# Performance work log

Hardware: AMD Instinct MI355X
Metric: run time of the kernel (lower is better)

The kernel has to match this reference:

```python
import jax, jax.numpy as jnp
import numpy as np

DIM = 384
HEADS = 12
WIN = (2, 7, 7)
MLP_RATIO = 4.0
EPS = 1e-5


def _rel_index(Wt, Wh, Ww):
    t, h, w = np.meshgrid(np.arange(Wt), np.arange(Wh), np.arange(Ww), indexing='ij')
    coords = np.stack([t, h, w]).reshape(3, -1).T  # (N,3)
    rel = coords[:, None] - coords[None]  # (N,N,3)
    rel[..., 0] += Wt - 1
    rel[..., 1] += Wh - 1
    rel[..., 2] += Ww - 1
    rel[..., 0] *= (2 * Wh - 1) * (2 * Ww - 1)
    rel[..., 1] *= (2 * Ww - 1)
    return rel.sum(-1)  # (N,N) int


def setup_inputs() -> dict:
    key = jax.random.key(0)
    ks = jax.random.split(key, 16)
    d = DIM
    hdim = int(d * MLP_RATIO)
    Wt, Wh, Ww = WIN
    table_size = (2 * Wt - 1) * (2 * Wh - 1) * (2 * Ww - 1)
    s = lambda fan: 1.0 / np.sqrt(fan)
    return {
        'x': jax.random.normal(ks[0], (2, 8, 56, 56, d), jnp.float32),
        'norm1_g': jnp.ones((d,), jnp.float32),
        'norm1_b': jnp.zeros((d,), jnp.float32),
        'qkv_w': jax.random.normal(ks[1], (d, 3 * d), jnp.float32) * s(d),
        'qkv_b': jnp.zeros((3 * d,), jnp.float32),
        'proj_w': jax.random.normal(ks[2], (d, d), jnp.float32) * s(d),
        'proj_b': jnp.zeros((d,), jnp.float32),
        'bias_table': jax.random.normal(ks[3], (table_size, HEADS), jnp.float32) * 0.02,
        'norm2_g': jnp.ones((d,), jnp.float32),
        'norm2_b': jnp.zeros((d,), jnp.float32),
        'fc1_w': jax.random.normal(ks[4], (d, hdim), jnp.float32) * s(d),
        'fc1_b': jnp.zeros((hdim,), jnp.float32),
        'fc2_w': jax.random.normal(ks[5], (hdim, d), jnp.float32) * s(hdim),
        'fc2_b': jnp.zeros((d,), jnp.float32),
        'rel_index': jnp.asarray(_rel_index(*WIN), jnp.int32),
    }


def _ln(x, g, b):
    mu = x.mean(-1, keepdims=True)
    var = ((x - mu) ** 2).mean(-1, keepdims=True)
    return (x - mu) * jax.lax.rsqrt(var + EPS) * g + b


def _window_partition(x, win):
    B, T, H, W, C = x.shape
    Wt, Wh, Ww = win
    x = x.reshape(B, T // Wt, Wt, H // Wh, Wh, W // Ww, Ww, C)
    x = x.transpose(0, 1, 3, 5, 2, 4, 6, 7)
    return x.reshape(-1, Wt * Wh * Ww, C)


def _window_reverse(win_x, win, B, T, H, W):
    Wt, Wh, Ww = win
    C = win_x.shape[-1]
    x = win_x.reshape(B, T // Wt, H // Wh, W // Ww, Wt, Wh, Ww, C)
    x = x.transpose(0, 1, 4, 2, 5, 3, 6, 7)
    return x.reshape(B, T, H, W, C)


def reference(x, norm1_g, norm1_b, qkv_w, qkv_b, proj_w, proj_b, bias_table,
              norm2_g, norm2_b, fc1_w, fc1_b, fc2_w, fc2_b, rel_index):
    B, T, H, W, C = x.shape
    Wt, Wh, Ww = WIN
    N = Wt * Wh * Ww
    shift = (Wt // 2, Wh // 2, Ww // 2)
    head_dim = C // HEADS
    scale = head_dim ** -0.5

    shortcut = x
    h = _ln(x, norm1_g, norm1_b)
    h = jnp.roll(h, shift=(-shift[0], -shift[1], -shift[2]), axis=(1, 2, 3))
    # dims chosen divisible by window -> no padding branch
    wins = _window_partition(h, WIN)  # (BnW, N, C)
    BnW = wins.shape[0]

    qkv = wins @ qkv_w + qkv_b  # (BnW, N, 3C)
    qkv = qkv.reshape(BnW, N, 3, HEADS, head_dim).transpose(2, 0, 3, 1, 4)
    q, k, v = qkv[0] * scale, qkv[1], qkv[2]  # (BnW, H, N, d)

    bias = bias_table[rel_index.reshape(-1)].reshape(N, N, HEADS).transpose(2, 0, 1)
    attn = jnp.einsum('bhnd,bhmd->bhnm', q, k) + bias[None]
    attn = jax.nn.softmax(attn, axis=-1)
    out = jnp.einsum('bhnm,bhmd->bhnd', attn, v)
    out = out.transpose(0, 2, 1, 3).reshape(BnW, N, C)
    out = out @ proj_w + proj_b

    h = _window_reverse(out.reshape(-1, Wt, Wh, Ww, C), WIN, B, T, H, W)
    h = jnp.roll(h, shift=shift, axis=(1, 2, 3))
    x = shortcut + h

    h2 = _ln(x, norm2_g, norm2_b)
    h2 = jax.nn.gelu(h2 @ fc1_w + fc1_b, approximate=False) @ fc2_w + fc2_b
    return x + h2
```

## Files before the change

### kernel.cpp

```cpp
#include <hip/hip_runtime.h>
#include <cstdint>
#include <cstddef>


typedef __bf16 bf16x8 __attribute__((ext_vector_type(8)));
typedef __bf16 bf16x4 __attribute__((ext_vector_type(4)));
typedef float f32x4 __attribute__((ext_vector_type(4)));

#define DIM 384
#define QKV_DIM 1152
#define HID 1536
#define NHEADS 12
#define NTOK 50176
#define NWIN 512

__device__ __forceinline__ void gload16(const void* g, void* s) {
  __builtin_amdgcn_global_load_lds(
      (const __attribute__((address_space(1))) void*)g,
      (__attribute__((address_space(3))) void*)s, 16, 0, 0);
}

__global__ __launch_bounds__(256) void build_tokmap_k(int* __restrict__ map) {
  int t = blockIdx.x * 256 + threadIdx.x;
  if (t >= NTOK) return;
  int win = t / 98, n = t - win * 98;
  int b = win >> 8, tw = (win >> 6) & 3, hw = (win >> 3) & 7, ww = win & 7;
  int dt = n / 49; int rem = n - dt * 49; int dh = rem / 7, dw = rem - dh * 7;
  int t0 = (tw * 2 + dt + 1) & 7;
  int h0 = hw * 7 + dh + 3; if (h0 >= 56) h0 -= 56;
  int w0 = ww * 7 + dw + 3; if (w0 >= 56) w0 -= 56;
  map[t] = ((b * 8 + t0) * 56 + h0) * 56 + w0;
}

__global__ __launch_bounds__(256) void expand_biasp_k(const float* __restrict__ table,
                                                      const int* __restrict__ rel,
                                                      float* __restrict__ out) {
  int e = blockIdx.x * 256 + threadIdx.x;
  if (e >= NHEADS * 49 * 256) return;
  int r = e & 3, l = (e >> 2) & 63;
  int rest = e >> 8;
  int ni = rest % 7, mi = (rest / 7) % 7, h = rest / 49;
  int i = mi * 16 + (l >> 4) * 4 + r;
  int j = ni * 16 + (l & 15);
  float v;
  if (j >= 98) v = -1e30f;
  else if (i >= 98) v = 0.f;
  else v = table[rel[i * 98 + j] * NHEADS + h];
  out[e] = v;
}

__global__ __launch_bounds__(256) void pack_w64_k(const float* __restrict__ W,
                                                  __bf16* __restrict__ WP,
                                                  int K, int N, int nk,
                                                  int scaleCols, float scale) {
  int idx = blockIdx.x * 256 + threadIdx.x;
  if (idx >= (K * N) >> 3) return;
  int l = idx & 63, f = (idx >> 6) & 7;
  int rest = idx >> 9, kt = rest % nk, cn = rest / nk;
  int n = f >> 1, kk = f & 1;
  int col = cn * 64 + n * 16 + (l & 15);
  int k0 = kt * 64 + (kk * 4 + (l >> 4)) * 8;
  float sc = (col < scaleCols) ? scale : 1.0f;
  bf16x8 v;
  #pragma unroll
  for (int j = 0; j < 8; ++j)
    v[j] = (__bf16)(W[(size_t)(k0 + j) * N + col] * sc);
  *(bf16x8*)(WP + (size_t)idx * 8) = v;
}

__global__ __launch_bounds__(256) void pack_w96_k(const float* __restrict__ W,
                                                  __bf16* __restrict__ WP) {
  int idx = blockIdx.x * 256 + threadIdx.x;
  if (idx >= (HID * DIM) >> 3) return;
  int l = idx & 63, n = (idx >> 6) % 6;
  int j8 = (idx / 384) % 48, w = idx / 18432;
  int col = w * 96 + n * 16 + (l & 15);
  int k0 = j8 * 32 + (l >> 4) * 8;
  bf16x8 v;
  #pragma unroll
  for (int j = 0; j < 8; ++j)
    v[j] = (__bf16)W[(size_t)(k0 + j) * DIM + col];
  *(bf16x8*)(WP + (size_t)idx * 8) = v;
}

__global__ __launch_bounds__(256) void scale_bias_k(const float* __restrict__ b,
                                                    float* __restrict__ out,
                                                    int n, int scaleCols, float scale) {
  int e = blockIdx.x * 256 + threadIdx.x;
  if (e >= n) return;
  out[e] = b[e] * (e < scaleCols ? scale : 1.0f);
}

__global__ __launch_bounds__(384) void vtrans_k(const __bf16* __restrict__ qkv,
                                                __bf16* __restrict__ vt) {
  __shared__ __align__(1024) char T[98304];
  int win = blockIdx.x, t = threadIdx.x;
  const __bf16* base = qkv + (size_t)win * 98 * QKV_DIM + 768 + t;
  #pragma unroll
  for (int c = 0; c < 16; ++c) {
    bf16x8 pk;
    #pragma unroll
    for (int e2 = 0; e2 < 8; ++e2) {
      int tok = c * 8 + e2;
      pk[e2] = (tok < 98) ? base[(size_t)tok * QKV_DIM] : (__bf16)0.f;
    }
    *(bf16x8*)(T + t * 256 + ((c ^ (t & 15)) << 4)) = pk;
  }
  __syncthreads();
  char* wb = (char*)(vt + (size_t)win * 49152);
  #pragma unroll
  for (int i = 0; i < 16; ++i) {
    int g = i * 6144 + t * 16;
    int row = g >> 8, p = (g >> 4) & 15;
    bf16x8 v = *(const bf16x8*)(T + row * 256 + (p << 4));
    int lc = p ^ (row & 15);
    *(bf16x8*)(wb + row * 256 + (lc << 4)) = v;
  }
}

template <typename T, bool MAP>
__global__ __launch_bounds__(256) void ln_pack_k(const T* __restrict__ x,
                                                 const float* __restrict__ g,
                                                 const float* __restrict__ bta,
                                                 __bf16* __restrict__ outp,
                                                 const int* __restrict__ map) {
  const int w = threadIdx.x >> 6, l = threadIdx.x & 63;
  const int tok = blockIdx.x * 32 + w * 8 + (l >> 3);
  const int src = MAP ? map[tok] : tok;
  const T* row = x + (size_t)src * DIM;
  const int o0 = l & 7;
  float v[6][8];
  float s = 0.f;
  #pragma unroll
  for (int j = 0; j < 6; ++j) {
    const int c = (o0 + 8 * j) * 8;
    if constexpr (sizeof(T) == 4) {
      f32x4 p0 = *(const f32x4*)(row + c);
      f32x4 p1 = *(const f32x4*)(row + c + 4);
      #pragma unroll
      for (int e = 0; e < 4; ++e) { v[j][e] = p0[e]; v[j][e + 4] = p1[e]; }
    } else {
      bf16x8 p = *(const bf16x8*)(row + c);
      #pragma unroll
      for (int e = 0; e < 8; ++e) v[j][e] = (float)p[e];
    }
    #pragma unroll
    for (int e = 0; e < 8; ++e) s += v[j][e];
  }
  s += __shfl_xor(s, 1, 64); s += __shfl_xor(s, 2, 64); s += __shfl_xor(s, 4, 64);
  const float mu = s * (1.f / DIM);
  float var = 0.f;
  #pragma unroll
  for (int j = 0; j < 6; ++j)
    #pragma unroll
    for (int e = 0; e < 8; ++e) { float d = v[j][e] - mu; var += d * d; }
  var += __shfl_xor(var, 1, 64); var += __shfl_xor(var, 2, 64); var += __shfl_xor(var, 4, 64);
  const float rs = rsqrtf(var * (1.f / DIM) + 1e-5f);
  const int mg = tok >> 6, m = (tok >> 4) & 3, lr = tok & 15;
  const int kk = o0 >> 2, lg = o0 & 3;
  __bf16* dst = outp + (size_t)mg * 24576 + (m * 2 + kk) * 512 + (lg * 16 + lr) * 8;
  #pragma unroll
  for (int j = 0; j < 6; ++j) {
    const int c = (o0 + 8 * j) * 8;
    f32x4 g0 = *(const f32x4*)(g + c), g1 = *(const f32x4*)(g + c + 4);
    f32x4 b0 = *(const f32x4*)(bta + c), b1 = *(const f32x4*)(bta + c + 4);
    bf16x8 ov;
    #pragma unroll
    for (int e = 0; e < 4; ++e) {
      ov[e] = (__bf16)((v[j][e] - mu) * rs * g0[e] + b0[e]);
      ov[e + 4] = (__bf16)((v[j][e + 4] - mu) * rs * g1[e] + b1[e]);
    }
    *(bf16x8*)(dst + (size_t)j * 4096) = ov;
  }
}

template <int EPI, int NK>
__global__ __launch_bounds__(256) void gemm_stream_k(const __bf16* __restrict__ AP,
                                                     const __bf16* __restrict__ WP,
                                                     const float* __restrict__ bias,
                                                     int N,
                                                     __bf16* __restrict__ outb) {
  __shared__ __align__(1024) char lds[32768];
  const int tid = threadIdx.x;
  const int l = tid & 63, w = tid >> 6;
  const int lr = l & 15, lg = l >> 4;
  const int ntile = N >> 6;
  const int nwg = gridDim.x, qd = nwg >> 3, rm = nwg & 7;
  const int xcd = blockIdx.x & 7;
  const int wgid = (xcd < rm ? xcd * (qd + 1) : rm * (qd + 1) + (xcd - rm) * qd)
                   + (blockIdx.x >> 3);
  const int bm = wgid / ntile, bn = wgid - bm * ntile;
  const int mg = bm * 4 + w;
  const int m0 = mg << 6, n0 = bn << 6;
  const __bf16* pA = AP + (size_t)mg * (NK * 4096) + l * 8;
  const __bf16* pB = WP + (size_t)bn * (NK * 4096) + l * 8;

  bf16x8 a[2][8], b[2][8];
  f32x4 acc[4][4] = {};
  #pragma unroll
  for (int f = 0; f < 8; ++f) {
    a[0][f] = *(const bf16x8*)(pA + f * 512);
    b[0][f] = *(const bf16x8*)(pB + f * 512);
  }
  #pragma unroll
  for (int kt = 0; kt < NK; ++kt) {
    const int cur = kt & 1, nxt = cur ^ 1;
    if (kt < NK - 1) {
      const size_t ko = (size_t)(kt + 1) * 4096;
      #pragma unroll
      for (int f = 0; f < 8; ++f) {
        a[nxt][f] = *(const bf16x8*)(pA + ko + f * 512);
        b[nxt][f] = *(const bf16x8*)(pB + ko + f * 512);
      }
      asm volatile("s_waitcnt vmcnt(16)" ::: "memory");
    } else {
      asm volatile("s_waitcnt vmcnt(0)" ::: "memory");
    }
    __builtin_amdgcn_sched_barrier(0);
    __builtin_amdgcn_s_setprio(1);
    #pragma unroll
    for (int kk = 0; kk < 2; ++kk)
      #pragma unroll
      for (int m = 0; m < 4; ++m)
        #pragma unroll
        for (int n = 0; n < 4; ++n)
          acc[m][n] = __builtin_amdgcn_mfma_f32_16x16x32_bf16(
              b[cur][n * 2 + kk], a[cur][m * 2 + kk], acc[m][n], 0, 0, 0);
    __builtin_amdgcn_s_setprio(0);
  }

  char* abuf = lds + (w << 13);
  #pragma unroll
  for (int m = 0; m < 4; ++m) {
    const int row = (m << 4) + lr;
    #pragma unroll
    for (int n = 0; n < 4; ++n) {
      const int gcol = n0 + (n << 4) + (lg << 2);
      f32x4 a4 = acc[m][n] + *(const f32x4*)(bias + gcol);
      bf16x4 c;
      #pragma unroll
      for (int r = 0; r < 4; ++r) c[r] = (__bf16)a4[r];
      const int ch = (n << 1) + (lg >> 1);
      *(bf16x4*)(abuf + (row << 7) + ((ch ^ (row & 7)) << 4) + ((lg & 1) << 3)) = c;
    }
  }
  asm volatile("s_waitcnt lgkmcnt(0)" ::: "memory");
  __builtin_amdgcn_sched_barrier(0);
  #pragma unroll
  for (int i = 0; i < 8; ++i) {
    const int row = (i << 3) + (l >> 3);
    const int p = (l & 7) ^ (row & 7);
    bf16x8 v = *(const bf16x8*)(abuf + (row << 7) + (p << 4));
    *(bf16x8*)(outb + (size_t)(m0 + row) * N + n0 + ((l & 7) << 3)) = v;
  }
}

__global__ __launch_bounds__(256, 2) void mlp_fused_k(const __bf16* __restrict__ AP,
                                                      const __bf16* __restrict__ W1P,
                                                      const float* __restrict__ b1,
                                                      const __bf16* __restrict__ W2P,
                                                      const float* __restrict__ b2,
                                                      const __bf16* __restrict__ s1,
                                                      float* __restrict__ outp) {
  __shared__ __align__(1024) char lds[81920];
  const int tid = threadIdx.x, l = tid & 63, w = tid >> 6;
  const int lr = l & 15, lg = l >> 4;
  const int bid = (blockIdx.x & 7) * (gridDim.x >> 3) + (blockIdx.x >> 3);
  const int tok0 = bid << 6;

  const __bf16* APg = AP + (size_t)bid * 24576;
  #pragma unroll
  for (int i = 0; i < 12; ++i) {
    const int c = w * 12 + i;
    gload16(APg + c * 512 + l * 8, lds + c * 1024);
  }
  asm volatile("s_waitcnt vmcnt(0)" ::: "memory");
  asm volatile("s_barrier" ::: "memory");

  char* hbase = lds + 49152;
  char* hb = hbase + (w << 13);
  const __bf16* W2w = W2P + (size_t)w * 147456 + l * 8;
  f32x4 acc2[4][6] = {};

#define LOADW2(dst, j, t)                                                      \
  { _Pragma("unroll")                                                          \
    for (int q_ = 0; q_ < 2; ++q_)                                             \
      _Pragma("unroll")                                                        \
      for (int n_ = 0; n_ < 6; ++n_)                                           \
        dst[q_ * 6 + n_] = *(const bf16x8*)(                                   \
            W2w + (size_t)(((j) * 8 + 2 * (t) + q_) * 6 + n_) * 512); }
#define FC2_STEP(T, BCUR, BNXT)                                                \
  {                                                                            \
    if ((T) < 3) LOADW2(BNXT, j, (T) + 1)                                      \
    bf16x8 ah[4][2];                                                           \
    const char* ht = hbase + ((T) << 13);                                      \
    _Pragma("unroll")                                                          \
    for (int m_ = 0; m_ < 4; ++m_)                                             \
      _Pragma("unroll")                                                        \
      for (int q_ = 0; q_ < 2; ++q_) {                                         \
        const int r_ = (m_ << 4) + lr, ck_ = (q_ << 2) + lg;                   \
        ah[m_][q_] = *(const bf16x8*)(ht + (r_ << 7) + ((ck_ ^ (r_ & 7)) << 4)); \
      }                                                                        \
    __builtin_amdgcn_s_setprio(1);                                             \
    _Pragma("unroll")                                                          \
    for (int q_ = 0; q_ < 2; ++q_)                                             \
      _Pragma("unroll")                                                        \
      for (int m_ = 0; m_ < 4; ++m_)                                           \
        _Pragma("unroll")                                                      \
        for (int n_ = 0; n_ < 6; ++n_)                                         \
          acc2[m_][n_] = __builtin_amdgcn_mfma_f32_16x16x32_bf16(              \
              BCUR[q_ * 6 + n_], ah[m_][q_], acc2[m_][n_], 0, 0, 0);           \
    __builtin_amdgcn_s_setprio(0);                                             \
  }

  for (int j = 0; j < 6; ++j) {
    const int g = j * 4 + w;
    const __bf16* W1g = W1P + (size_t)g * 24576 + l * 8;
    f32x4 acc1[4][4] = {};
    #pragma unroll
    for (int kt = 0; kt < 6; ++kt) {
      bf16x8 a[4][2], b[8];
      #pragma unroll
      for (int f = 0; f < 8; ++f)
        b[f] = *(const bf16x8*)(W1g + kt * 4096 + f * 512);
      #pragma unroll
      for (int m = 0; m < 4; ++m)
        #pragma unroll
        for (int kk = 0; kk < 2; ++kk)
          a[m][kk] = *(const bf16x8*)(lds + (kt * 8 + m * 2 + kk) * 1024 + l * 16);
      __builtin_amdgcn_s_setprio(1);
      #pragma unroll
      for (int kk = 0; kk < 2; ++kk)
        #pragma unroll
        for (int m = 0; m < 4; ++m)
          #pragma unroll
          for (int n = 0; n < 4; ++n)
            acc1[m][n] = __builtin_amdgcn_mfma_f32_16x16x32_bf16(
                b[n * 2 + kk], a[m][kk], acc1[m][n], 0, 0, 0);
      __builtin_amdgcn_s_setprio(0);
    }
    asm volatile("s_barrier" ::: "memory");
    #pragma unroll
    for (int m = 0; m < 4; ++m) {
      const int row = (m << 4) + lr;
      #pragma unroll
      for (int n = 0; n < 4; ++n) {
        f32x4 a4 = acc1[m][n] + *(const f32x4*)(b1 + g * 64 + (n << 4) + (lg << 2));
        bf16x4 c;
        #pragma unroll
        for (int r = 0; r < 4; ++r) {
          float vv = a4[r];
          float y = vv * (1.0f + 0.044715f * vv * vv);
          c[r] = (__bf16)(vv / (1.0f + __expf(-1.5957691216057308f * y)));
        }
        const int ch = (n << 1) + (lg >> 1);
        *(bf16x4*)(hb + (row << 7) + ((ch ^ (row & 7)) << 4) + ((lg & 1) << 3)) = c;
      }
    }
    asm volatile("s_waitcnt lgkmcnt(0)" ::: "memory");
    __builtin_amdgcn_sched_barrier(0);
    asm volatile("s_barrier" ::: "memory");
    {
      bf16x8 bhA[12], bhB[12];
      LOADW2(bhA, j, 0)
      FC2_STEP(0, bhA, bhB)
      FC2_STEP(1, bhB, bhA)
      FC2_STEP(2, bhA, bhB)
      FC2_STEP(3, bhB, bhA)
    }
  }
#undef FC2_STEP
#undef LOADW2

  const int col0 = w * 96;
  #pragma unroll
  for (int m = 0; m < 4; ++m) {
    const int grow = tok0 + (m << 4) + lr;
    #pragma unroll
    for (int n = 0; n < 6; ++n) {
      const int gcol = col0 + (n << 4) + (lg << 2);
      f32x4 a4 = acc2[m][n] + *(const f32x4*)(b2 + gcol);
      bf16x4 sv = *(const bf16x4*)(s1 + (size_t)grow * DIM + gcol);
      f32x4 o;
      #pragma unroll
      for (int r = 0; r < 4; ++r) o[r] = a4[r] + (float)sv[r];
      *(f32x4*)(outp + (size_t)grow * DIM + gcol) = o;
    }
  }
}

__global__ __launch_bounds__(256) void gemm_proj_k(const __bf16* __restrict__ A,
                                                   const __bf16* __restrict__ WP,
                                                   const float* __restrict__ bias,
                                                   int M, int N, int K,
                                                   __bf16* __restrict__ outb,
                                                   const float* __restrict__ residf,
                                                   const int* __restrict__ tokmap) {
  __shared__ __align__(1024) char lds[32768];
  const int tid = threadIdx.x;
  const int l = tid & 63, w = tid >> 6;
  const int lr = l & 15, lg = l >> 4;
  const int ntile = N >> 6;
  const int nwg = gridDim.x, qd = nwg >> 3, rm = nwg & 7;
  const int xcd = blockIdx.x & 7;
  const int wgid = (xcd < rm ? xcd * (qd + 1) : rm * (qd + 1) + (xcd - rm) * qd)
                   + (blockIdx.x >> 3);
  const int bm = wgid / ntile, bn = wgid - bm * ntile;
  const int m0 = (bm << 8) + (w << 6);
  const int n0 = bn << 6;
  const int nk = K >> 6;
  const int sch = (l & 7) ^ ((l >> 3) & 7);
  const __bf16* pa = A + (size_t)(m0 + (l >> 3)) * K + sch * 8;
  char* abuf = lds + (w << 13);
  const __bf16* pB = WP + (size_t)bn * nk * 4096 + l * 8;

#define STAGEA(kt)                                                   \
  { const size_t ko_ = (size_t)(kt) << 6;                            \
    _Pragma("unroll")                                                \
    for (int s_ = 0; s_ < 8; ++s_)                                   \
      gload16(pa + (size_t)(s_ * 8) * K + ko_, abuf + s_ * 1024); }
#define LOADB(kt)                                                    \
  { const __bf16* p_ = pB + (size_t)(kt) * 4096;                     \
    _Pragma("unroll")                                                \
    for (int f_ = 0; f_ < 8; ++f_)                                   \
      b[f_] = *(const bf16x8*)(p_ + f_ * 512); }
#define LDA()                                                        \
  { _Pragma("unroll")                                                \
    for (int kk_ = 0; kk_ < 2; ++kk_) {                              \
      const int ck_ = (kk_ << 2) + lg;                               \
      _Pragma("unroll")                                              \
      for (int m_ = 0; m_ < 4; ++m_) {                               \
        int r_ = (m_ << 4) + lr;                                     \
        a[m_][kk_] = *(const bf16x8*)(abuf + (r_ << 7) +             \
                                      ((ck_ ^ (r_ & 7)) << 4));      \
      } }                                                            \
    asm volatile("s_waitcnt lgkmcnt(0)" ::: "memory");               \
    __builtin_amdgcn_sched_barrier(0); }

  bf16x8 a[4][2], b[8];
  f32x4 acc[4][4] = {};
  STAGEA(0)
  asm volatile("s_waitcnt vmcnt(0)" ::: "memory");
  LDA()
  for (int kt = 0; kt < nk; ++kt) {
    LOADB(kt)
    const bool pf = (kt + 1 < nk);
    if (pf) STAGEA(kt + 1)
    __builtin_amdgcn_s_setprio(1);
    #pragma unroll
    for (int kk = 0; kk < 2; ++kk)
      #pragma unroll
      for (int m = 0; m < 4; ++m)
        #pragma unroll
        for (int n = 0; n < 4; ++n)
          acc[m][n] = __builtin_amdgcn_mfma_f32_16x16x32_bf16(b[n * 2 + kk], a[m][kk],
                                                              acc[m][n], 0, 0, 0);
    __builtin_amdgcn_s_setprio(0);
    if (pf) {
      asm volatile("s_waitcnt vmcnt(0)" ::: "memory");
      LDA()
    }
  }
#undef STAGEA
#undef LOADB
#undef LDA

  #pragma unroll
  for (int m = 0; m < 4; ++m) {
    const int row = (m << 4) + lr;
    #pragma unroll
    for (int n = 0; n < 4; ++n) {
      const int gcol = n0 + (n << 4) + (lg << 2);
      f32x4 a4 = acc[m][n] + *(const f32x4*)(bias + gcol);
      bf16x4 c;
      #pragma unroll
      for (int r = 0; r < 4; ++r) c[r] = (__bf16)a4[r];
      const int ch = (n << 1) + (lg >> 1);
      *(bf16x4*)(abuf + (row << 7) + ((ch ^ (row & 7)) << 4) + ((lg & 1) << 3)) = c;
    }
  }
  asm volatile("s_waitcnt lgkmcnt(0)" ::: "memory");
  __builtin_amdgcn_sched_barrier(0);
  #pragma unroll
  for (int i = 0; i < 8; ++i) {
    const int row = (i << 3) + (l >> 3);
    const int p = (l & 7) ^ (row & 7);
    bf16x8 v = *(const bf16x8*)(abuf + (row << 7) + (p << 4));
    const int gcol = n0 + ((l & 7) << 3);
    const int dst = tokmap[m0 + row];
    const float* rp = residf + (size_t)dst * N + gcol;
    f32x4 r0 = *(const f32x4*)rp, r1 = *(const f32x4*)(rp + 4);
    bf16x8 c2;
    #pragma unroll
    for (int j = 0; j < 4; ++j) {
      c2[j] = (__bf16)(r0[j] + (float)v[j]);
      c2[j + 4] = (__bf16)(r1[j] + (float)v[j + 4]);
    }
    *(bf16x8*)(outb + (size_t)dst * N + gcol) = c2;
  }
}

__global__ __launch_bounds__(64) void attn_k(const __bf16* __restrict__ qkv,
                                             const __bf16* __restrict__ vt,
                                             const float* __restrict__ pb,
                                             __bf16* __restrict__ out) {
  __shared__ __align__(1024) char P[4096];
  const int l = threadIdx.x, lr = l & 15, lg = l >> 4;
  const int bid = blockIdx.x;
  const int xc = bid & 7, kk = bid >> 3;
  const int wh = (kk / 7) * 8 + xc, mi = kk % 7;
  const int win = wh / NHEADS, h = wh - win * NHEADS;
  const size_t wbase = (size_t)win * 98 * QKV_DIM;
  const __bf16* qb = qkv + wbase + h * 32;
  const __bf16* kb = qb + 384;
  const bf16x8 z8 = {};
  const f32x4 fz = {};

  bf16x8 kf[7];
  #pragma unroll
  for (int ni = 0; ni < 7; ++ni) {
    int tok = ni * 16 + lr;
    kf[ni] = (tok < 98) ? *(const bf16x8*)(kb + (size_t)tok * QKV_DIM + lg * 8) : z8;
  }
  int qt = mi * 16 + lr;
  bf16x8 qf = (qt < 98) ? *(const bf16x8*)(qb + (size_t)qt * QKV_DIM + lg * 8) : z8;
  const f32x4* pbp = (const f32x4*)pb + (size_t)((h * 7 + mi) * 7) * 64 + l;
  f32x4 bv[7];
  #pragma unroll
  for (int ni = 0; ni < 7; ++ni) bv[ni] = pbp[ni * 64];

  f32x4 s[7];
  #pragma unroll
  for (int ni = 0; ni < 7; ++ni)
    s[ni] = __builtin_amdgcn_mfma_f32_16x16x32_bf16(qf, kf[ni], fz, 0, 0, 0);

  if (l < 32) {
    int row = l >> 1, c = 14 + (l & 1);
    *(f32x4*)(P + row * 256 + ((c ^ (row & 7)) << 4)) = fz;
  }

  #pragma unroll
  for (int r = 0; r < 4; ++r) {
    float mx = -1e30f;
    #pragma unroll
    for (int ni = 0; ni < 7; ++ni) {
      float vv = s[ni][r] + bv[ni][r];
      s[ni][r] = vv;
      mx = fmaxf(mx, vv);
    }
    #pragma unroll
    for (int m2 = 1; m2 < 16; m2 <<= 1) mx = fmaxf(mx, __shfl_xor(mx, m2, 64));
    float sum = 0.f;
    #pragma unroll
    for (int ni = 0; ni < 7; ++ni) { float p = __expf(s[ni][r] - mx); s[ni][r] = p; sum += p; }
    #pragma unroll
    for (int m2 = 1; m2 < 16; m2 <<= 1) sum += __shfl_xor(sum, m2, 64);
    float inv = 1.0f / sum;
    int il = lg * 4 + r;
    #pragma unroll
    for (int ni = 0; ni < 7; ++ni) {
      int j = ni * 16 + lr;
      *(__bf16*)(P + il * 256 + (((j >> 3) ^ (il & 7)) << 4) + ((j & 7) << 1)) =
          (__bf16)(s[ni][r] * inv);
    }
  }
  __syncthreads();

  bf16x8 pa[4];
  #pragma unroll
  for (int ks = 0; ks < 4; ++ks) {
    int ck = ks * 4 + lg;
    pa[ks] = *(const bf16x8*)(P + lr * 256 + ((ck ^ (lr & 7)) << 4));
  }
  const __bf16* vrow = vt + ((size_t)wh * 32) * 128;
  f32x4 oo[2];
  #pragma unroll
  for (int nf = 0; nf < 2; ++nf) {
    int d = nf * 16 + lr;
    f32x4 o = fz;
    #pragma unroll
    for (int ks = 0; ks < 4; ++ks) {
      bf16x8 vb = *(const bf16x8*)(vrow + (size_t)d * 128 + ks * 32 + lg * 8);
      o = __builtin_amdgcn_mfma_f32_16x16x32_bf16(pa[ks], vb, o, 0, 0, 0);
    }
    oo[nf] = o;
  }
  #pragma unroll
  for (int nf = 0; nf < 2; ++nf)
    #pragma unroll
    for (int r = 0; r < 4; ++r)
      *(__bf16*)(P + (lg * 4 + r) * 64 + (((nf << 4) + lr) << 1)) = (__bf16)oo[nf][r];
  asm volatile("s_waitcnt lgkmcnt(0)" ::: "memory");
  __builtin_amdgcn_sched_barrier(0);
  {
    const int row = l >> 2;
    bf16x8 v = *(const bf16x8*)(P + row * 64 + ((l & 3) << 4));
    const int tok = mi * 16 + row;
    if (tok < 98)
      *(bf16x8*)(out + ((size_t)win * 98 + tok) * DIM + h * 32 + ((l & 3) << 3)) = v;
  }
}

extern "C" void kernel_launch(void* const* d_in, const int* in_sizes, int n_in,
                              void* d_out, int out_size, void* d_ws, size_t ws_size,
                              hipStream_t stream) {
  const float* x      = (const float*)d_in[0];
  const float* n1g    = (const float*)d_in[1];
  const float* n1b    = (const float*)d_in[2];
  const float* qkv_w  = (const float*)d_in[3];
  const float* qkv_b  = (const float*)d_in[4];
  const float* proj_w = (const float*)d_in[5];
  const float* proj_b = (const float*)d_in[6];
  const float* btab   = (const float*)d_in[7];
  const float* n2g    = (const float*)d_in[8];
  const float* n2b    = (const float*)d_in[9];
  const float* fc1_w  = (const float*)d_in[10];
  const float* fc1_b  = (const float*)d_in[11];
  const float* fc2_w  = (const float*)d_in[12];
  const float* fc2_b  = (const float*)d_in[13];
  const int*   relidx = (const int*)d_in[14];
  float* outp = (float*)d_out;
  (void)in_sizes; (void)n_in; (void)out_size; (void)ws_size;

  char* ws = (char*)d_ws;
  size_t off = 0;
  auto alloc = [&](size_t bytes) {
    char* p = ws + off;
    off = (off + bytes + 255) & ~(size_t)255;
    return p;
  };
  int*    tokmap  = (int*)alloc((size_t)NTOK * 4);
  float*  biasex  = (float*)alloc((size_t)NHEADS * 49 * 256 * 4);
  __bf16* wqkvP   = (__bf16*)alloc((size_t)QKV_DIM * DIM * 2);
  __bf16* wprojP  = (__bf16*)alloc((size_t)DIM * DIM * 2);
  __bf16* wfc1P   = (__bf16*)alloc((size_t)HID * DIM * 2);
  __bf16* wfc2P   = (__bf16*)alloc((size_t)DIM * HID * 2);
  float*  qkvbS   = (float*)alloc((size_t)QKV_DIM * 4);
  __bf16* tokens  = (__bf16*)alloc((size_t)NTOK * DIM * 2);
  __bf16* qkvbuf  = (__bf16*)alloc((size_t)NTOK * HID * 2);
  __bf16* s1      = (__bf16*)alloc((size_t)NTOK * DIM * 2);
  __bf16* tokens2 = (__bf16*)alloc((size_t)NTOK * DIM * 2);
  __bf16* attnout = tokens;
  __bf16* vt = (__bf16*)d_out;

  const float scale = 0.17677669529663687f;

  build_tokmap_k<<<NTOK / 256, 256, 0, stream>>>(tokmap);
  expand_biasp_k<<<(NHEADS * 49 * 256) / 256, 256, 0, stream>>>(btab, relidx, biasex);
  pack_w64_k<<<(DIM * QKV_DIM / 8) / 256, 256, 0, stream>>>(qkv_w, wqkvP, DIM, QKV_DIM, 6, DIM, scale);
  pack_w64_k<<<(DIM * DIM / 8) / 256, 256, 0, stream>>>(proj_w, wprojP, DIM, DIM, 6, 0, 1.0f);
  pack_w64_k<<<(DIM * HID / 8) / 256, 256, 0, stream>>>(fc1_w, wfc1P, DIM, HID, 6, 0, 1.0f);
  pack_w96_k<<<(HID * DIM / 8) / 256, 256, 0, stream>>>(fc2_w, wfc2P);
  scale_bias_k<<<(QKV_DIM + 255) / 256, 256, 0, stream>>>(qkv_b, qkvbS, QKV_DIM, DIM, scale);

  ln_pack_k<float, true><<<NTOK / 32, 256, 0, stream>>>(x, n1g, n1b, tokens, tokmap);
  gemm_stream_k<0, 6><<<(NTOK / 256) * (QKV_DIM / 64), 256, 0, stream>>>(
      tokens, wqkvP, qkvbS, QKV_DIM, qkvbuf);
  vtrans_k<<<NWIN, 384, 0, stream>>>(qkvbuf, vt);
  attn_k<<<NWIN * NHEADS * 7, 64, 0, stream>>>(qkvbuf, vt, biasex, attnout);
  gemm_proj_k<<<(NTOK / 256) * (DIM / 64), 256, 0, stream>>>(
      attnout, wprojP, proj_b, NTOK, DIM, DIM, s1, x, tokmap);
  ln_pack_k<__bf16, false><<<NTOK / 32, 256, 0, stream>>>(s1, n2g, n2b, tokens2, nullptr);
  mlp_fused_k<<<NTOK / 64, 256, 0, stream>>>(
      tokens2, wfc1P, fc1_b, wfc2P, fc2_b, s1, outp);
}
```

Baseline: 450.6 us.

## Fuse LN2 into MLP kernel and write attention output in packed GEMM layout

The attention kernel now writes its output directly in the pre-packed tile layout that the streaming GEMM consumes. This lets the projection reuse gemm_stream_k with a residual-scatter epilogue instead of the separate gemm_proj_k that staged A through LDS. The standalone second LayerNorm pack kernel is removed: mlp_fused_k reads s1 rows, computes mean and variance, and writes the normalized bf16 tile straight into LDS. This saves one kernel launch and a full-size write and read of the intermediate tensor, at the cost of extra register pressure and latency in the MLP prologue.

```diff
diff --git a/kernel.cpp b/kernel.cpp
--- a/kernel.cpp
+++ b/kernel.cpp
@@ -179,7 +179,9 @@
                                                      const __bf16* __restrict__ WP,
                                                      const float* __restrict__ bias,
                                                      int N,
-                                                     __bf16* __restrict__ outb) {
+                                                     __bf16* __restrict__ outb,
+                                                     const float* __restrict__ residf,
+                                                     const int* __restrict__ tokmap) {
   __shared__ __align__(1024) char lds[32768];
   const int tid = threadIdx.x;
   const int l = tid & 63, w = tid >> 6;
@@ -251,16 +253,31 @@
     const int row = (i << 3) + (l >> 3);
     const int p = (l & 7) ^ (row & 7);
     bf16x8 v = *(const bf16x8*)(abuf + (row << 7) + (p << 4));
-    *(bf16x8*)(outb + (size_t)(m0 + row) * N + n0 + ((l & 7) << 3)) = v;
-  }
-}
-
-__global__ __launch_bounds__(256, 2) void mlp_fused_k(const __bf16* __restrict__ AP,
+    const int gcol = n0 + ((l & 7) << 3);
+    if (EPI == 1) {
+      const int dst = tokmap[m0 + row];
+      const float* rp = residf + (size_t)dst * N + gcol;
+      f32x4 r0 = *(const f32x4*)rp, r1 = *(const f32x4*)(rp + 4);
+      bf16x8 c2;
+      #pragma unroll
+      for (int j = 0; j < 4; ++j) {
+        c2[j] = (__bf16)(r0[j] + (float)v[j]);
+        c2[j + 4] = (__bf16)(r1[j] + (float)v[j + 4]);
+      }
+      *(bf16x8*)(outb + (size_t)dst * N + gcol) = c2;
+    } else {
+      *(bf16x8*)(outb + (size_t)(m0 + row) * N + gcol) = v;
+    }
+  }
+}
+
+__global__ __launch_bounds__(256, 2) void mlp_fused_k(const __bf16* __restrict__ s1,
+                                                      const float* __restrict__ g2,
+                                                      const float* __restrict__ bt2,
                                                       const __bf16* __restrict__ W1P,
                                                       const float* __restrict__ b1,
                                                       const __bf16* __restrict__ W2P,
                                                       const float* __restrict__ b2,
-                                                      const __bf16* __restrict__ s1,
                                                       float* __restrict__ outp) {
   __shared__ __align__(1024) char lds[81920];
   const int tid = threadIdx.x, l = tid & 63, w = tid >> 6;
@@ -268,14 +285,47 @@
   const int bid = (blockIdx.x & 7) * (gridDim.x >> 3) + (blockIdx.x >> 3);
   const int tok0 = bid << 6;
 
-  const __bf16* APg = AP + (size_t)bid * 24576;
-  #pragma unroll
-  for (int i = 0; i < 12; ++i) {
-    const int c = w * 12 + i;
-    gload16(APg + c * 512 + l * 8, lds + c * 1024);
-  }
-  asm volatile("s_waitcnt vmcnt(0)" ::: "memory");
-  asm volatile("s_barrier" ::: "memory");
+  {
+    const int rloc = (w << 4) + (l >> 2);
+    const int p = l & 3;
+    const __bf16* srow = s1 + (size_t)(tok0 + rloc) * DIM;
+    float vv[12][8];
+    float s = 0.f;
+    #pragma unroll
+    for (int j = 0; j < 12; ++j) {
+      const int o = (j << 2) + p;
+      bf16x8 pk = *(const bf16x8*)(srow + (o << 3));
+      #pragma unroll
+      for (int e = 0; e < 8; ++e) { vv[j][e] = (float)pk[e]; s += vv[j][e]; }
+    }
+    s += __shfl_xor(s, 1, 64); s += __shfl_xor(s, 2, 64);
+    const float mu = s * (1.f / DIM);
+    float var = 0.f;
+    #pragma unroll
+    for (int j = 0; j < 12; ++j)
+      #pragma unroll
+      for (int e = 0; e < 8; ++e) { float d = vv[j][e] - mu; var += d * d; }
+    var += __shfl_xor(var, 1, 64); var += __shfl_xor(var, 2, 64);
+    const float rs = rsqrtf(var * (1.f / DIM) + 1e-5f);
+    const int m2 = rloc >> 4, lr2 = rloc & 15;
+    #pragma unroll
+    for (int j = 0; j < 12; ++j) {
+      const int o = (j << 2) + p;
+      const int kt = o >> 3, kk2 = (o >> 2) & 1, lg2 = o & 3;
+      f32x4 g0 = *(const f32x4*)(g2 + (o << 3));
+      f32x4 g1 = *(const f32x4*)(g2 + (o << 3) + 4);
+      f32x4 b0 = *(const f32x4*)(bt2 + (o << 3));
+      f32x4 b1 = *(const f32x4*)(bt2 + (o << 3) + 4);
+      bf16x8 ov;
+      #pragma unroll
+      for (int e = 0; e < 4; ++e) {
+        ov[e] = (__bf16)((vv[j][e] - mu) * rs * g0[e] + b0[e]);
+        ov[e + 4] = (__bf16)((vv[j][e + 4] - mu) * rs * g1[e] + b1[e]);
+      }
+      *(bf16x8*)(lds + (kt * 8 + m2 * 2 + kk2) * 1024 + ((lg2 << 4) + lr2) * 16) = ov;
+    }
+  }
+  __syncthreads();
 
   char* hbase = lds + 49152;
   char* hb = hbase + (w << 13);
@@ -349,9 +399,9 @@
         bf16x4 c;
         #pragma unroll
         for (int r = 0; r < 4; ++r) {
-          float vv = a4[r];
-          float y = vv * (1.0f + 0.044715f * vv * vv);
-          c[r] = (__bf16)(vv / (1.0f + __expf(-1.5957691216057308f * y)));
+          float vvv = a4[r];
+          float y = vvv * (1.0f + 0.044715f * vvv * vvv);
+          c[r] = (__bf16)(vvv / (1.0f + __expf(-1.5957691216057308f * y)));
         }
         const int ch = (n << 1) + (lg >> 1);
         *(bf16x4*)(hb + (row << 7) + ((ch ^ (row & 7)) << 4) + ((lg & 1) << 3)) = c;
@@ -389,121 +439,10 @@
   }
 }
 
-__global__ __launch_bounds__(256) void gemm_proj_k(const __bf16* __restrict__ A,
-                                                   const __bf16* __restrict__ WP,
-                                                   const float* __restrict__ bias,
-                                                   int M, int N, int K,
-                                                   __bf16* __restrict__ outb,
-                                                   const float* __restrict__ residf,
-                                                   const int* __restrict__ tokmap) {
-  __shared__ __align__(1024) char lds[32768];
-  const int tid = threadIdx.x;
-  const int l = tid & 63, w = tid >> 6;
-  const int lr = l & 15, lg = l >> 4;
-  const int ntile = N >> 6;
-  const int nwg = gridDim.x, qd = nwg >> 3, rm = nwg & 7;
-  const int xcd = blockIdx.x & 7;
-  const int wgid = (xcd < rm ? xcd * (qd + 1) : rm * (qd + 1) + (xcd - rm) * qd)
-                   + (blockIdx.x >> 3);
-  const int bm = wgid / ntile, bn = wgid - bm * ntile;
-  const int m0 = (bm << 8) + (w << 6);
-  const int n0 = bn << 6;
-  const int nk = K >> 6;
-  const int sch = (l & 7) ^ ((l >> 3) & 7);
-  const __bf16* pa = A + (size_t)(m0 + (l >> 3)) * K + sch * 8;
-  char* abuf = lds + (w << 13);
-  const __bf16* pB = WP + (size_t)bn * nk * 4096 + l * 8;
-
-#define STAGEA(kt)                                                   \
-  { const size_t ko_ = (size_t)(kt) << 6;                            \
-    _Pragma("unroll")                                                \
-    for (int s_ = 0; s_ < 8; ++s_)                                   \
-      gload16(pa + (size_t)(s_ * 8) * K + ko_, abuf + s_ * 1024); }
-#define LOADB(kt)                                                    \
-  { const __bf16* p_ = pB + (size_t)(kt) * 4096;                     \
-    _Pragma("unroll")                                                \
-    for (int f_ = 0; f_ < 8; ++f_)                                   \
-      b[f_] = *(const bf16x8*)(p_ + f_ * 512); }
-#define LDA()                                                        \
-  { _Pragma("unroll")                                                \
-    for (int kk_ = 0; kk_ < 2; ++kk_) {                              \
-      const int ck_ = (kk_ << 2) + lg;                               \
-      _Pragma("unroll")                                              \
-      for (int m_ = 0; m_ < 4; ++m_) {                               \
-        int r_ = (m_ << 4) + lr;                                     \
-        a[m_][kk_] = *(const bf16x8*)(abuf + (r_ << 7) +             \
-                                      ((ck_ ^ (r_ & 7)) << 4));      \
-      } }                                                            \
-    asm volatile("s_waitcnt lgkmcnt(0)" ::: "memory");               \
-    __builtin_amdgcn_sched_barrier(0); }
-
-  bf16x8 a[4][2], b[8];
-  f32x4 acc[4][4] = {};
-  STAGEA(0)
-  asm volatile("s_waitcnt vmcnt(0)" ::: "memory");
-  LDA()
-  for (int kt = 0; kt < nk; ++kt) {
-    LOADB(kt)
-    const bool pf = (kt + 1 < nk);
-    if (pf) STAGEA(kt + 1)
-    __builtin_amdgcn_s_setprio(1);
-    #pragma unroll
-    for (int kk = 0; kk < 2; ++kk)
-      #pragma unroll
-      for (int m = 0; m < 4; ++m)
-        #pragma unroll
-        for (int n = 0; n < 4; ++n)
-          acc[m][n] = __builtin_amdgcn_mfma_f32_16x16x32_bf16(b[n * 2 + kk], a[m][kk],
-                                                              acc[m][n], 0, 0, 0);
-    __builtin_amdgcn_s_setprio(0);
-    if (pf) {
-      asm volatile("s_waitcnt vmcnt(0)" ::: "memory");
-      LDA()
-    }
-  }
-#undef STAGEA
-#undef LOADB
-#undef LDA
-
-  #pragma unroll
-  for (int m = 0; m < 4; ++m) {
-    const int row = (m << 4) + lr;
-    #pragma unroll
-    for (int n = 0; n < 4; ++n) {
-      const int gcol = n0 + (n << 4) + (lg << 2);
-      f32x4 a4 = acc[m][n] + *(const f32x4*)(bias + gcol);
-      bf16x4 c;
-      #pragma unroll
-      for (int r = 0; r < 4; ++r) c[r] = (__bf16)a4[r];
-      const int ch = (n << 1) + (lg >> 1);
-      *(bf16x4*)(abuf + (row << 7) + ((ch ^ (row & 7)) << 4) + ((lg & 1) << 3)) = c;
-    }
-  }
-  asm volatile("s_waitcnt lgkmcnt(0)" ::: "memory");
-  __builtin_amdgcn_sched_barrier(0);
-  #pragma unroll
-  for (int i = 0; i < 8; ++i) {
-    const int row = (i << 3) + (l >> 3);
-    const int p = (l & 7) ^ (row & 7);
-    bf16x8 v = *(const bf16x8*)(abuf + (row << 7) + (p << 4));
-    const int gcol = n0 + ((l & 7) << 3);
-    const int dst = tokmap[m0 + row];
-    const float* rp = residf + (size_t)dst * N + gcol;
-    f32x4 r0 = *(const f32x4*)rp, r1 = *(const f32x4*)(rp + 4);
-    bf16x8 c2;
-    #pragma unroll
-    for (int j = 0; j < 4; ++j) {
-      c2[j] = (__bf16)(r0[j] + (float)v[j]);
-      c2[j + 4] = (__bf16)(r1[j] + (float)v[j + 4]);
-    }
-    *(bf16x8*)(outb + (size_t)dst * N + gcol) = c2;
-  }
-}
-
 __global__ __launch_bounds__(64) void attn_k(const __bf16* __restrict__ qkv,
                                              const __bf16* __restrict__ vt,
                                              const float* __restrict__ pb,
-                                             __bf16* __restrict__ out) {
+                                             __bf16* __restrict__ outp) {
   __shared__ __align__(1024) char P[4096];
   const int l = threadIdx.x, lr = l & 15, lg = l >> 4;
   const int bid = blockIdx.x;
@@ -596,8 +535,14 @@
     const int row = l >> 2;
     bf16x8 v = *(const bf16x8*)(P + row * 64 + ((l & 3) << 4));
     const int tok = mi * 16 + row;
-    if (tok < 98)
-      *(bf16x8*)(out + ((size_t)win * 98 + tok) * DIM + h * 32 + ((l & 3) << 3)) = v;
+    if (tok < 98) {
+      const int tg = win * 98 + tok;
+      const int o = (h << 2) + (l & 3);
+      const int mg2 = tg >> 6, m2 = (tg >> 4) & 3, lr2 = tg & 15;
+      const int kt = o >> 3, kk2 = (o >> 2) & 1, lg2 = o & 3;
+      *(bf16x8*)(outp + (size_t)mg2 * 24576 +
+                 ((size_t)((kt * 8 + m2 * 2 + kk2) * 64 + (lg2 << 4) + lr2)) * 8) = v;
+    }
   }
 }
 
@@ -639,8 +584,6 @@
   __bf16* tokens  = (__bf16*)alloc((size_t)NTOK * DIM * 2);
   __bf16* qkvbuf  = (__bf16*)alloc((size_t)NTOK * HID * 2);
   __bf16* s1      = (__bf16*)alloc((size_t)NTOK * DIM * 2);
-  __bf16* tokens2 = (__bf16*)alloc((size_t)NTOK * DIM * 2);
-  __bf16* attnout = tokens;
   __bf16* vt = (__bf16*)d_out;
 
   const float scale = 0.17677669529663687f;
@@ -655,12 +598,11 @@
 
   ln_pack_k<float, true><<<NTOK / 32, 256, 0, stream>>>(x, n1g, n1b, tokens, tokmap);
   gemm_stream_k<0, 6><<<(NTOK / 256) * (QKV_DIM / 64), 256, 0, stream>>>(
-      tokens, wqkvP, qkvbS, QKV_DIM, qkvbuf);
+      tokens, wqkvP, qkvbS, QKV_DIM, qkvbuf, nullptr, nullptr);
   vtrans_k<<<NWIN, 384, 0, stream>>>(qkvbuf, vt);
-  attn_k<<<NWIN * NHEADS * 7, 64, 0, stream>>>(qkvbuf, vt, biasex, attnout);
-  gemm_proj_k<<<(NTOK / 256) * (DIM / 64), 256, 0, stream>>>(
-      attnout, wprojP, proj_b, NTOK, DIM, DIM, s1, x, tokmap);
-  ln_pack_k<__bf16, false><<<NTOK / 32, 256, 0, stream>>>(s1, n2g, n2b, tokens2, nullptr);
+  attn_k<<<NWIN * NHEADS * 7, 64, 0, stream>>>(qkvbuf, vt, biasex, tokens);
+  gemm_stream_k<1, 6><<<(NTOK / 256) * (DIM / 64), 256, 0, stream>>>(
+      tokens, wprojP, proj_b, DIM, s1, x, tokmap);
   mlp_fused_k<<<NTOK / 64, 256, 0, stream>>>(
-      tokens2, wfc1P, fc1_b, wfc2P, fc2_b, s1, outp);
-}
+      s1, n2g, n2b, wfc1P, fc1_b, wfc2P, fc2_b, outp);
+}
```

Result: no change. 441.8 us, median of 2 (-2.0%).
